# Kernel optimization log

Measured on AMD Instinct MI355X. Metric: run time of the kernel, lower is better.

Reference implementation:

```python
import jax, jax.numpy as jnp
import numpy as np

B, N, E, FIMG = 8, 10242, 61440, 512


def setup_inputs() -> dict:
    key = jax.random.key(0)
    ks = jax.random.split(key, 16)
    inp = {
        "batch_vertices": jax.random.normal(ks[0], (B, N, 3), jnp.float32),
        "img_features": jax.random.normal(ks[1], (B, FIMG), jnp.float32),
        "edge_indices": jax.random.randint(ks[2], (2, E), 0, N, dtype=jnp.int32),
    }
    dims = [(3 + FIMG, 512), (512, 512), (512, 512), (512, 512), (512, 64), (64, 3)]
    for i, (fi, fo) in enumerate(dims, 1):
        inp[f"W{i}"] = jax.random.normal(ks[2 + i], (fi, fo), jnp.float32) / np.sqrt(fi).astype(np.float32)
        inp[f"b{i}"] = jnp.zeros((fo,), jnp.float32)
    return inp


def _gcn(x, W, b, src, dst, norm, n):
    # GCNConv: h = x @ W ; out[i] = sum_{(j->i)} norm_e * h[j] ; + b
    h = jnp.einsum('bnf,fo->bno', x, W)
    msg = h[:, src, :] * norm[None, :, None]        # [B, E+N, Fo]
    out = jnp.zeros((x.shape[0], n, W.shape[1]), x.dtype).at[:, dst, :].add(msg)
    return out + b


def reference(batch_vertices, img_features, edge_indices,
              W1, b1, W2, b2, W3, b3, W4, b4, W5, b5, W6, b6):
    n = batch_vertices.shape[1]
    loop = jnp.arange(n, dtype=edge_indices.dtype)
    src = jnp.concatenate([edge_indices[0], loop])  # add self-loops (GCN)
    dst = jnp.concatenate([edge_indices[1], loop])
    deg = jnp.zeros((n,), jnp.float32).at[dst].add(1.0)
    dinv = jnp.where(deg > 0, jax.lax.rsqrt(deg), 0.0)
    norm = dinv[src] * dinv[dst]                    # symmetric normalization

    feat = jnp.broadcast_to(img_features[:, None, :], (batch_vertices.shape[0], n, img_features.shape[1]))
    x = jnp.concatenate([batch_vertices, feat], axis=2)

    x = _gcn(x, W1, b1, src, dst, norm, n)
    x = _gcn(x, W2, b2, src, dst, norm, n)
    x = jax.nn.relu(x)
    x = _gcn(x, W3, b3, src, dst, norm, n)
    x = _gcn(x, W4, b4, src, dst, norm, n)
    x = jax.nn.relu(x)
    x = _gcn(x, W5, b5, src, dst, norm, n)
    x = _gcn(x, W6, b6, src, dst, norm, n)
    return x
```

## Files before the change

kernel.cpp:

```cpp
#include <hip/hip_runtime.h>
#include <hip/hip_bf16.h>

typedef __attribute__((ext_vector_type(8))) short short8_t;
typedef __attribute__((ext_vector_type(4))) float f32x4;

#define DEV __device__ __forceinline__

constexpr int BB = 8;
constexpr int NV = 10242;
constexpr int NE = 61440;
constexpr int MROWS = BB * NV;
constexpr int KD = 512;

DEV float bf2f(ushort u) { union { unsigned i; float f; } v; v.i = ((unsigned)u) << 16; return v.f; }
DEV ushort f2bf(float f) {
    union { unsigned i; float f; } v; v.f = f;
    unsigned b = v.i;
    b += 0x7fffu + ((b >> 16) & 1u);
    return (ushort)(b >> 16);
}

__global__ void k_init(int* deg, int* fill) {
    int i = blockIdx.x * 256 + threadIdx.x;
    if (i < NV) { deg[i] = 1; fill[i] = 0; }
}

__global__ void k_count(const int* __restrict__ ei, int* __restrict__ deg) {
    int e = blockIdx.x * 256 + threadIdx.x;
    if (e < NE) atomicAdd(&deg[ei[NE + e]], 1);
}

__global__ __launch_bounds__(1024) void k_scan(const int* __restrict__ cnt, int* __restrict__ rp) {
    __shared__ int part[1024];
    const int t = threadIdx.x;
    const int chunk = (NV + 1023) / 1024;
    int b0 = t * chunk, b1 = min(b0 + chunk, NV);
    int s = 0;
    for (int i = b0; i < b1; ++i) s += cnt[i];
    part[t] = s;
    __syncthreads();
    for (int off = 1; off < 1024; off <<= 1) {
        int v = (t >= off) ? part[t - off] : 0;
        __syncthreads();
        part[t] += v;
        __syncthreads();
    }
    int run = (t == 0) ? 0 : part[t - 1];
    for (int i = b0; i < b1; ++i) { rp[i] = run; run += cnt[i]; }
    if (t == 1023) rp[NV] = part[1023];
}

__global__ void k_fill(const int* __restrict__ ei, const int* __restrict__ rp,
                       int* __restrict__ fill, const int* __restrict__ deg,
                       int* __restrict__ ci, float* __restrict__ val) {
    int e = blockIdx.x * 256 + threadIdx.x;
    if (e >= NE + NV) return;
    int s, d;
    if (e < NE) { s = ei[e]; d = ei[NE + e]; }
    else        { s = d = e - NE; }
    int p = atomicAdd(&fill[d], 1);
    int pos = rp[d] + p;
    ci[pos] = s;
    val[pos] = rsqrtf((float)deg[s]) * rsqrtf((float)deg[d]);
}

__global__ __launch_bounds__(256) void k_aggsc(const float* __restrict__ src, float* __restrict__ dst,
                                               const int* __restrict__ rp, const int* __restrict__ ci,
                                               const float* __restrict__ val,
                                               const float* __restrict__ sin, float* __restrict__ sout,
                                               int gMR_) {
    const int bid = blockIdx.x;
    if (bid < gMR_) {
        int idx = bid * 256 + threadIdx.x;
        if (idx >= MROWS) return;
        int b = idx / NV, i = idx - b * NV;
        float a0 = 0.f, a1 = 0.f, a2 = 0.f;
        const float* sb = src + (size_t)b * NV * 3;
        for (int e = rp[i]; e < rp[i + 1]; ++e) {
            int j = ci[e];
            float wv = val[e];
            a0 = fmaf(wv, sb[j * 3 + 0], a0);
            a1 = fmaf(wv, sb[j * 3 + 1], a1);
            a2 = fmaf(wv, sb[j * 3 + 2], a2);
        }
        float* o = dst + ((size_t)b * NV + i) * 3;
        o[0] = a0; o[1] = a1; o[2] = a2;
    } else {
        int i = (bid - gMR_) * 256 + threadIdx.x;
        if (i >= NV) return;
        float a = 0.f;
        if (sin) { for (int e = rp[i]; e < rp[i + 1]; ++e) a = fmaf(val[e], sin[ci[e]], a); }
        else     { for (int e = rp[i]; e < rp[i + 1]; ++e) a += val[e]; }
        sout[i] = a;
    }
}

__global__ __launch_bounds__(256) void k_prep(const float* __restrict__ W4, const float* __restrict__ W3,
                                              const float* __restrict__ W5, const float* __restrict__ W1,
                                              const float* __restrict__ b1, const float* __restrict__ b3,
                                              const float* __restrict__ W2, const float* __restrict__ img,
                                              ushort* __restrict__ Wt4, ushort* __restrict__ W3c,
                                              ushort* __restrict__ Wt5, float* __restrict__ CW12,
                                              float* __restrict__ b1w2, float* __restrict__ b3w4,
                                              float* __restrict__ basev) {
    constexpr int WB = (2 * 512 * 512 + 64 * 512) / 256;
    const int bid = blockIdx.x;
    const int t = threadIdx.x;
    if (bid < WB) {
        int idx = bid * 256 + t;
        if (idx < 512 * 512) {
            int n = idx >> 9, k = idx & 511;
            Wt4[idx] = f2bf(W4[k * 512 + n]);
        } else if (idx < 2 * 512 * 512) {
            int j = idx - 512 * 512;
            W3c[j] = f2bf(W3[j]);
        } else {
            int j = idx - 2 * 512 * 512;
            int n = j >> 9, k = j & 511;
            Wt5[j] = f2bf(W5[k * 64 + n]);
        }
    } else if (bid < WB + 10) {
        int r = bid - WB;
        int y = r >> 1;
        int c = (r & 1) * 256 + t;
        const float* Mrow = (y < 3) ? (W1 + y * 512) : (y == 3 ? b1 : b3);
        const float* W = (y < 4) ? W2 : W4;
        float a = 0.f;
        for (int k = 0; k < 512; ++k) a = fmaf(Mrow[k], W[(size_t)k * 512 + c], a);
        float* o = (y < 3) ? (CW12 + y * 512) : (y == 3 ? b1w2 : b3w4);
        o[c] = a;
    } else {
        int r = bid - (WB + 10);
        int b = r >> 1;
        int c = (r & 1) * 256 + t;
        float s = 0.f;
        for (int k = 0; k < 512; ++k) s = fmaf(img[b * 512 + k], W1[(size_t)(3 + k) * 512 + c], s);
        basev[b * 512 + c] = s;
    }
}

__global__ __launch_bounds__(128) void k_matvecs(const float* __restrict__ M, const float* __restrict__ W,
                                                 float* __restrict__ out) {
    int c = blockIdx.x * 128 + threadIdx.x;
    int r = blockIdx.y;
    float a = 0.f;
    for (int k = 0; k < 512; ++k) a = fmaf(M[r * 512 + k], W[(size_t)k * 512 + c], a);
    out[r * 512 + c] = a;
}

__global__ __launch_bounds__(256) void k_x2(const float* __restrict__ aggV2, const float* __restrict__ s,
                                            const float* __restrict__ s2, const float* __restrict__ CW12,
                                            const float* __restrict__ bw2, const float* __restrict__ b1w2,
                                            const float* __restrict__ b2, ushort* __restrict__ r2) {
    const int t = threadIdx.x;
    int row = blockIdx.x * 2 + (t >> 7);
    if (row >= MROWS) return;
    int i = row >> 3, b = row & 7;
    const float* av = aggV2 + ((size_t)b * NV + i) * 3;
    float a0 = av[0], a1 = av[1], a2 = av[2];
    float si = s[i], s2i = s2[i];
    int c = (t & 127) * 4;
    float4 w0 = *(const float4*)&CW12[c];
    float4 w1 = *(const float4*)&CW12[512 + c];
    float4 w2 = *(const float4*)&CW12[1024 + c];
    float4 bw = *(const float4*)&bw2[b * 512 + c];
    float4 bv = *(const float4*)&b1w2[c];
    float4 b2v = *(const float4*)&b2[c];
    float o0 = a0 * w0.x + a1 * w1.x + a2 * w2.x + s2i * bw.x + si * bv.x + b2v.x;
    float o1 = a0 * w0.y + a1 * w1.y + a2 * w2.y + s2i * bw.y + si * bv.y + b2v.y;
    float o2 = a0 * w0.z + a1 * w1.z + a2 * w2.z + s2i * bw.z + si * bv.z + b2v.z;
    float o3 = a0 * w0.w + a1 * w1.w + a2 * w2.w + s2i * bw.w + si * bv.w + b2v.w;
    ushort4 o;
    o.x = f2bf(fmaxf(o0, 0.f));
    o.y = f2bf(fmaxf(o1, 0.f));
    o.z = f2bf(fmaxf(o2, 0.f));
    o.w = f2bf(fmaxf(o3, 0.f));
    *(ushort4*)&r2[(size_t)row * 512 + c] = o;
}

#define WAITVM(n) do { \
    asm volatile("s_waitcnt vmcnt(" #n ")" ::: "memory"); \
    __builtin_amdgcn_sched_barrier(0); \
    __builtin_amdgcn_s_barrier(); \
    __builtin_amdgcn_sched_barrier(0); \
} while (0)

template <int EPI>
__global__ __launch_bounds__(256) void k_gemm(const ushort* __restrict__ A, const ushort* __restrict__ Bt,
                                              ushort* __restrict__ C, int Mr, int Nc,
                                              const float* __restrict__ sv, const float* __restrict__ eb1,
                                              const float* __restrict__ eb2) {
    const int ncb = (Nc + 127) >> 7;
    const int nrc = (Mr + 127) >> 7;
    const int cpx = (nrc + 7) >> 3;
    const int bid = blockIdx.x;
    const int xcd = bid & 7;
    const int k = bid >> 3;
    const int rc = xcd * cpx + k / ncb;
    const int cb = k % ncb;
    if (rc >= nrc) return;

    __shared__ __align__(16) ushort lA[3][4096];
    __shared__ __align__(16) ushort lB[3][4096];
    const int t = threadIdx.x;
    const int lane = t & 63, w = t >> 6;
    const int wr = w >> 1, wc = w & 1;
    const int r0 = rc * 128, c0 = cb * 128;

    const ushort* gA[2]; const ushort* gB[2];
    int ldsoff[2];
    #pragma unroll
    for (int i2 = 0; i2 < 2; ++i2) {
        int idx = i2 * 256 + t;
        int row = idx >> 2, slot = idx & 3;
        int srcslot = slot ^ ((row >> 1) & 3);
        int ar = min(r0 + row, Mr - 1);
        int bc = min(c0 + row, Nc - 1);
        gA[i2] = A + (size_t)ar * KD + srcslot * 8;
        gB[i2] = Bt + (size_t)bc * KD + srcslot * 8;
        ldsoff[i2] = idx * 8;
    }

    auto stage = [&](int buf, int kt) {
        int ko = kt * 32;
        #pragma unroll
        for (int i2 = 0; i2 < 2; ++i2) {
            __builtin_amdgcn_global_load_lds(
                (const __attribute__((address_space(1))) void*)(gA[i2] + ko),
                (__attribute__((address_space(3))) void*)(&lA[buf][ldsoff[i2]]), 16, 0, 0);
            __builtin_amdgcn_global_load_lds(
                (const __attribute__((address_space(1))) void*)(gB[i2] + ko),
                (__attribute__((address_space(3))) void*)(&lB[buf][ldsoff[i2]]), 16, 0, 0);
        }
    };

    f32x4 acc[4][4] = {};
    const int rloc = lane & 15;
    const int kb = lane >> 4;
    const int kbs = (kb ^ ((rloc >> 1) & 3)) * 8;

    auto compute = [&](int buf) {
        short8_t af[4], bfr[4];
        #pragma unroll
        for (int m = 0; m < 4; ++m) {
            af[m]  = *(const short8_t*)&lA[buf][(wr * 64 + m * 16 + rloc) * 32 + kbs];
            bfr[m] = *(const short8_t*)&lB[buf][(wc * 64 + m * 16 + rloc) * 32 + kbs];
        }
        #pragma unroll
        for (int m = 0; m < 4; ++m)
            #pragma unroll
            for (int n = 0; n < 4; ++n)
                acc[m][n] = __builtin_amdgcn_mfma_f32_16x16x32_bf16(bfr[n], af[m], acc[m][n], 0, 0, 0);
    };

    stage(0, 0);
    stage(1, 1);
    WAITVM(4);
    int cur = 0;
    for (int kt = 0; kt < 14; ++kt) {
        int sb = cur + 2; if (sb > 2) sb -= 3;
        stage(sb, kt + 2);
        compute(cur);
        WAITVM(4);
        cur = (cur == 2) ? 0 : cur + 1;
    }
    compute(cur);
    WAITVM(0);
    cur = (cur == 2) ? 0 : cur + 1;
    compute(cur);

    #pragma unroll
    for (int m = 0; m < 4; ++m) {
        const int gr = r0 + wr * 64 + m * 16 + rloc;
        if (gr >= Mr) continue;
        #pragma unroll
        for (int n = 0; n < 4; ++n) {
            const int qc = c0 + wc * 64 + n * 16;
            if (qc >= Nc) continue;
            const int gc = qc + kb * 4;
            float v0 = acc[m][n][0], v1 = acc[m][n][1], v2 = acc[m][n][2], v3 = acc[m][n][3];
            if (EPI == 1) {
                const float s = sv[gr >> 3];
                const float4 e1 = *(const float4*)&eb1[gc];
                const float4 e2 = *(const float4*)&eb2[gc];
                v0 = fmaxf(v0 + s * e1.x + e2.x, 0.f);
                v1 = fmaxf(v1 + s * e1.y + e2.y, 0.f);
                v2 = fmaxf(v2 + s * e1.z + e2.z, 0.f);
                v3 = fmaxf(v3 + s * e1.w + e2.w, 0.f);
            }
            ushort4 o;
            o.x = f2bf(v0); o.y = f2bf(v1); o.z = f2bf(v2); o.w = f2bf(v3);
            *(ushort4*)&C[(size_t)gr * Nc + gc] = o;
        }
    }
}

__global__ __launch_bounds__(256) void k_gemm64(const ushort* __restrict__ A, const ushort* __restrict__ Bt,
                                                ushort* __restrict__ C) {
    const int rc = blockIdx.x;
    const int r0 = rc * 256;
    __shared__ __align__(16) ushort lA[2][8192];
    __shared__ __align__(16) ushort lB[2][2048];
    const int t = threadIdx.x;
    const int lane = t & 63, w = t >> 6;

    const ushort* gA[4]; int loffA[4];
    #pragma unroll
    for (int p = 0; p < 4; ++p) {
        int idx = p * 256 + t;
        int row = idx >> 2, slot = idx & 3;
        int srcslot = slot ^ ((row >> 1) & 3);
        int ar = min(r0 + row, MROWS - 1);
        gA[p] = A + (size_t)ar * KD + srcslot * 8;
        loffA[p] = idx * 8;
    }
    const int brow = t >> 2, bslot = (t & 3) ^ ((brow >> 1) & 3);
    const ushort* gB = Bt + (size_t)brow * KD + bslot * 8;
    const int loffB = t * 8;

    auto stage = [&](int buf, int kt) {
        int ko = kt * 32;
        #pragma unroll
        for (int p = 0; p < 4; ++p)
            __builtin_amdgcn_global_load_lds(
                (const __attribute__((address_space(1))) void*)(gA[p] + ko),
                (__attribute__((address_space(3))) void*)(&lA[buf][loffA[p]]), 16, 0, 0);
        __builtin_amdgcn_global_load_lds(
            (const __attribute__((address_space(1))) void*)(gB + ko),
            (__attribute__((address_space(3))) void*)(&lB[buf][loffB]), 16, 0, 0);
    };

    f32x4 acc[4][4] = {};
    stage(0, 0);
    __syncthreads();
    int cur = 0;
    const int rloc = lane & 15;
    const int kb = lane >> 4;
    const int kbs = (kb ^ ((rloc >> 1) & 3)) * 8;
    for (int kt = 0; kt < 16; ++kt) {
        if (kt < 15) stage(cur ^ 1, kt + 1);
        short8_t af[4], bfr[4];
        #pragma unroll
        for (int m = 0; m < 4; ++m) {
            af[m]  = *(const short8_t*)&lA[cur][(w * 64 + m * 16 + rloc) * 32 + kbs];
            bfr[m] = *(const short8_t*)&lB[cur][(m * 16 + rloc) * 32 + kbs];
        }
        #pragma unroll
        for (int m = 0; m < 4; ++m)
            #pragma unroll
            for (int n = 0; n < 4; ++n)
                acc[m][n] = __builtin_amdgcn_mfma_f32_16x16x32_bf16(bfr[n], af[m], acc[m][n], 0, 0, 0);
        __syncthreads();
        cur ^= 1;
    }

    #pragma unroll
    for (int m = 0; m < 4; ++m) {
        const int gr = r0 + w * 64 + m * 16 + rloc;
        if (gr >= MROWS) continue;
        #pragma unroll
        for (int n = 0; n < 4; ++n) {
            const int gc = n * 16 + kb * 4;
            ushort4 o;
            o.x = f2bf(acc[m][n][0]); o.y = f2bf(acc[m][n][1]);
            o.z = f2bf(acc[m][n][2]); o.w = f2bf(acc[m][n][3]);
            *(ushort4*)&C[(size_t)gr * 64 + gc] = o;
        }
    }
}

template <bool RELU>
__global__ __launch_bounds__(512) void k_aggv(const ushort* __restrict__ h, ushort* __restrict__ xo,
                                              const int* __restrict__ rp, const int* __restrict__ ci,
                                              const float* __restrict__ val) {
    constexpr int CH = BB * 512;
    const int i = blockIdx.x;
    const int t = threadIdx.x;
    const int r0 = rp[i], r1 = rp[i + 1];
    const ushort* hb = h + t * 8;
    float acc[8] = {};
    for (int e = r0; e < r1; e += 4) {
        const bool p1 = e + 1 < r1, p2 = e + 2 < r1, p3 = e + 3 < r1;
        const int j0 = ci[e];
        const int j1 = p1 ? ci[e + 1] : j0;
        const int j2 = p2 ? ci[e + 2] : j0;
        const int j3 = p3 ? ci[e + 3] : j0;
        const float w0 = val[e];
        const float w1 = p1 ? val[e + 1] : 0.f;
        const float w2 = p2 ? val[e + 2] : 0.f;
        const float w3 = p3 ? val[e + 3] : 0.f;
        const short8_t v0 = *(const short8_t*)(hb + (size_t)j0 * CH);
        const short8_t v1 = *(const short8_t*)(hb + (size_t)j1 * CH);
        const short8_t v2 = *(const short8_t*)(hb + (size_t)j2 * CH);
        const short8_t v3 = *(const short8_t*)(hb + (size_t)j3 * CH);
        #pragma unroll
        for (int k = 0; k < 8; ++k) {
            float a = acc[k];
            a = fmaf(w0, bf2f((ushort)v0[k]), a);
            a = fmaf(w1, bf2f((ushort)v1[k]), a);
            a = fmaf(w2, bf2f((ushort)v2[k]), a);
            a = fmaf(w3, bf2f((ushort)v3[k]), a);
            acc[k] = a;
        }
    }
    short8_t o;
    #pragma unroll
    for (int k = 0; k < 8; ++k) {
        float a = acc[k];
        if (RELU) a = fmaxf(a, 0.f);
        o[k] = (short)f2bf(a);
    }
    *(short8_t*)(xo + (size_t)i * CH + t * 8) = o;
}

__global__ __launch_bounds__(64) void k_aggv64f(const ushort* __restrict__ h, float* __restrict__ h3,
                                                const int* __restrict__ rp, const int* __restrict__ ci,
                                                const float* __restrict__ val, const float* __restrict__ b5,
                                                const float* __restrict__ W6) {
    constexpr int CH = BB * 64;
    __shared__ float w6[192];
    const int t = threadIdx.x;
    w6[t] = W6[t]; w6[t + 64] = W6[t + 64]; w6[t + 128] = W6[t + 128];
    __syncthreads();
    const int i = blockIdx.x;
    const int r0 = rp[i], r1 = rp[i + 1];
    const ushort* hb = h + t * 8;
    float acc[8] = {};
    for (int e = r0; e < r1; e += 4) {
        const bool p1 = e + 1 < r1, p2 = e + 2 < r1, p3 = e + 3 < r1;
        const int j0 = ci[e];
        const int j1 = p1 ? ci[e + 1] : j0;
        const int j2 = p2 ? ci[e + 2] : j0;
        const int j3 = p3 ? ci[e + 3] : j0;
        const float w0 = val[e];
        const float w1 = p1 ? val[e + 1] : 0.f;
        const float w2 = p2 ? val[e + 2] : 0.f;
        const float w3 = p3 ? val[e + 3] : 0.f;
        const short8_t v0 = *(const short8_t*)(hb + (size_t)j0 * CH);
        const short8_t v1 = *(const short8_t*)(hb + (size_t)j1 * CH);
        const short8_t v2 = *(const short8_t*)(hb + (size_t)j2 * CH);
        const short8_t v3 = *(const short8_t*)(hb + (size_t)j3 * CH);
        #pragma unroll
        for (int k = 0; k < 8; ++k) {
            float a = acc[k];
            a = fmaf(w0, bf2f((ushort)v0[k]), a);
            a = fmaf(w1, bf2f((ushort)v1[k]), a);
            a = fmaf(w2, bf2f((ushort)v2[k]), a);
            a = fmaf(w3, bf2f((ushort)v3[k]), a);
            acc[k] = a;
        }
    }
    const int fb = (t & 7) * 8;
    float p0 = 0.f, p1 = 0.f, p2 = 0.f;
    #pragma unroll
    for (int k = 0; k < 8; ++k) {
        float a = acc[k] + b5[fb + k];
        p0 = fmaf(a, w6[(fb + k) * 3 + 0], p0);
        p1 = fmaf(a, w6[(fb + k) * 3 + 1], p1);
        p2 = fmaf(a, w6[(fb + k) * 3 + 2], p2);
    }
    p0 += __shfl_xor(p0, 1); p0 += __shfl_xor(p0, 2); p0 += __shfl_xor(p0, 4);
    p1 += __shfl_xor(p1, 1); p1 += __shfl_xor(p1, 2); p1 += __shfl_xor(p1, 4);
    p2 += __shfl_xor(p2, 1); p2 += __shfl_xor(p2, 2); p2 += __shfl_xor(p2, 4);
    if ((t & 7) == 0) {
        int row = i * 8 + (t >> 3);
        float* o = h3 + (size_t)row * 3;
        o[0] = p0; o[1] = p1; o[2] = p2;
    }
}

__global__ __launch_bounds__(256) void k_agg3(const float* __restrict__ h3, float* __restrict__ out,
                                              const int* __restrict__ rp, const int* __restrict__ ci,
                                              const float* __restrict__ val, const float* __restrict__ b6) {
    int idx = blockIdx.x * 256 + threadIdx.x;
    if (idx >= MROWS) return;
    int b = idx / NV, i = idx - b * NV;
    float a0 = b6[0], a1 = b6[1], a2 = b6[2];
    int r0 = rp[i], r1 = rp[i + 1];
    for (int e = r0; e < r1; ++e) {
        int j = ci[e];
        float wv = val[e];
        const float* hr = h3 + ((size_t)j * BB + b) * 3;
        a0 = fmaf(wv, hr[0], a0);
        a1 = fmaf(wv, hr[1], a1);
        a2 = fmaf(wv, hr[2], a2);
    }
    float* o = out + (size_t)idx * 3;
    o[0] = a0; o[1] = a1; o[2] = a2;
}

extern "C" void kernel_launch(void* const* d_in, const int* in_sizes, int n_in,
                              void* d_out, int out_size, void* d_ws, size_t ws_size,
                              hipStream_t stream) {
    const float* verts = (const float*)d_in[0];
    const float* img   = (const float*)d_in[1];
    const int*   ei    = (const int*)d_in[2];
    const float* W1 = (const float*)d_in[3];  const float* b1 = (const float*)d_in[4];
    const float* W2 = (const float*)d_in[5];  const float* b2 = (const float*)d_in[6];
    const float* W3 = (const float*)d_in[7];  const float* b3 = (const float*)d_in[8];
    const float* W4 = (const float*)d_in[9];  const float* b4 = (const float*)d_in[10];
    const float* W5 = (const float*)d_in[11]; const float* b5 = (const float*)d_in[12];
    const float* W6 = (const float*)d_in[13]; const float* b6 = (const float*)d_in[14];
    float* out = (float*)d_out;

    char* ws = (char*)d_ws;
    size_t off = 0;
    auto carve = [&](size_t bytes) -> void* {
        void* q = ws + off;
        off += (bytes + 255) & ~(size_t)255;
        return q;
    };
    ushort* bufA = (ushort*)carve((size_t)MROWS * 512 * 2);
    ushort* bufB = (ushort*)carve((size_t)MROWS * 512 * 2);
    ushort* Wt4  = (ushort*)carve((size_t)512 * 512 * 2);
    ushort* W3c  = (ushort*)carve((size_t)512 * 512 * 2);
    ushort* Wt34 = (ushort*)carve((size_t)512 * 512 * 2);
    ushort* Wt5  = (ushort*)carve((size_t)64 * 512 * 2);
    float*  basev = (float*)carve((size_t)BB * 512 * 4);
    float*  bw2   = (float*)carve((size_t)BB * 512 * 4);
    float*  CW12  = (float*)carve((size_t)3 * 512 * 4);
    float*  b1w2  = (float*)carve((size_t)512 * 4);
    float*  b3w4  = (float*)carve((size_t)512 * 4);
    int*    deg  = (int*)carve((size_t)NV * 4);
    int*    fill = (int*)carve((size_t)NV * 4);
    float*  sV   = (float*)carve((size_t)NV * 4);
    float*  s2V  = (float*)carve((size_t)NV * 4);
    int*    rp   = (int*)carve((size_t)(NV + 1) * 4);
    int*    ci   = (int*)carve((size_t)(NE + NV) * 4);
    float*  valv = (float*)carve((size_t)(NE + NV) * 4);
    float*  aggV  = (float*)carve((size_t)MROWS * 3 * 4);
    float*  aggV2 = (float*)carve((size_t)MROWS * 3 * 4);
    float*  h3   = (float*)carve((size_t)MROWS * 3 * 4);

    dim3 b256(256);
    const int gNV = (NV + 255) / 256;
    const int gMR = (MROWS + 255) / 256;
    k_init<<<dim3(gNV), b256, 0, stream>>>(deg, fill);
    k_count<<<dim3((NE + 255) / 256), b256, 0, stream>>>(ei, deg);
    k_scan<<<dim3(1), dim3(1024), 0, stream>>>(deg, rp);
    k_fill<<<dim3((NE + NV + 255) / 256), b256, 0, stream>>>(ei, rp, fill, deg, ci, valv);
    k_aggsc<<<dim3(gMR + gNV), b256, 0, stream>>>(verts, aggV, rp, ci, valv, nullptr, sV, gMR);
    k_aggsc<<<dim3(gMR + gNV), b256, 0, stream>>>(aggV, aggV2, rp, ci, valv, sV, s2V, gMR);
    k_prep<<<dim3(2176 + 10 + 16), b256, 0, stream>>>(W4, W3, W5, W1, b1, b3, W2, img,
                                                      Wt4, W3c, Wt5, CW12, b1w2, b3w4, basev);
    k_matvecs<<<dim3(4, BB), dim3(128), 0, stream>>>(basev, W2, bw2);
    k_gemm<0><<<dim3(32), b256, 0, stream>>>(Wt4, W3c, Wt34, 512, 512, nullptr, nullptr, nullptr);
    k_x2<<<dim3((MROWS + 1) / 2), b256, 0, stream>>>(aggV2, sV, s2V, CW12, bw2, b1w2, b2, bufA);
    k_aggv<false><<<dim3(NV), dim3(512), 0, stream>>>(bufA, bufB, rp, ci, valv);
    k_aggv<false><<<dim3(NV), dim3(512), 0, stream>>>(bufB, bufA, rp, ci, valv);
    const int nrc = (MROWS + 127) / 128;
    const int g512 = 8 * ((nrc + 7) / 8) * 4;
    k_gemm<1><<<dim3(g512), b256, 0, stream>>>(bufA, Wt34, bufB, MROWS, 512, sV, b3w4, b4);
    k_gemm64<<<dim3((MROWS + 255) / 256), b256, 0, stream>>>(bufB, Wt5, bufA);
    k_aggv64f<<<dim3(NV), dim3(64), 0, stream>>>(bufA, h3, rp, ci, valv, b5, W6);
    k_agg3<<<dim3(gMR), b256, 0, stream>>>(h3, out, rp, ci, valv, b6);
}
```

Baseline: 455.2 us.

## Split sparse aggregation into XCD-pinned column panels for L2 locality

Replaces the one-block-per-vertex 512-thread aggregation with 256-thread blocks that each handle 16 vertices over one 128-column panel of the 4096-wide row. Panels are assigned by block index modulo 8 so each XCD keeps working on the same column slice. The aim is for neighbor gathers to hit in that XCD's L2 instead of pulling full 8KB rows across all dies. Each vertex's CSR indices and weights are now read once per panel (32 times) instead of once, and per-vertex edge-loop divergence within a wave rises.

After: 391.4 us (median of 2 runs). -14.0%, faster.

```diff
diff --git a/kernel.cpp b/kernel.cpp
--- a/kernel.cpp
+++ b/kernel.cpp
@@ -9,6 +9,7 @@
 constexpr int BB = 8;
 constexpr int NV = 10242;
 constexpr int NE = 61440;
+constexpr int NET = NE + NV;
 constexpr int MROWS = BB * NV;
 constexpr int KD = 512;
 
@@ -54,7 +55,7 @@
                        int* __restrict__ fill, const int* __restrict__ deg,
                        int* __restrict__ ci, float* __restrict__ val) {
     int e = blockIdx.x * 256 + threadIdx.x;
-    if (e >= NE + NV) return;
+    if (e >= NET) return;
     int s, d;
     if (e < NE) { s = ei[e]; d = ei[NE + e]; }
     else        { s = d = e - NE; }
@@ -369,15 +370,22 @@
     }
 }
 
-template <bool RELU>
-__global__ __launch_bounds__(512) void k_aggv(const ushort* __restrict__ h, ushort* __restrict__ xo,
-                                              const int* __restrict__ rp, const int* __restrict__ ci,
-                                              const float* __restrict__ val) {
-    constexpr int CH = BB * 512;
-    const int i = blockIdx.x;
-    const int t = threadIdx.x;
+constexpr int NVG16 = (NV + 15) / 16;
+__global__ __launch_bounds__(256) void k_aggvp(const ushort* __restrict__ h, ushort* __restrict__ xo,
+                                               const int* __restrict__ rp, const int* __restrict__ ci,
+                                               const float* __restrict__ val) {
+    const int bid = blockIdx.x;
+    const int xcd = bid & 7;
+    const int g = bid >> 3;
+    const int round = g / NVG16;
+    const int vg = g - round * NVG16;
+    const int panel = xcd + round * 8;
+    const int t = threadIdx.x;
+    const int i = vg * 16 + (t >> 4);
+    if (i >= NV) return;
+    const int po = panel * 128 + (t & 15) * 8;
+    const ushort* hb = h + po;
     const int r0 = rp[i], r1 = rp[i + 1];
-    const ushort* hb = h + t * 8;
     float acc[8] = {};
     for (int e = r0; e < r1; e += 4) {
         const bool p1 = e + 1 < r1, p2 = e + 2 < r1, p3 = e + 3 < r1;
@@ -389,10 +397,10 @@
         const float w1 = p1 ? val[e + 1] : 0.f;
         const float w2 = p2 ? val[e + 2] : 0.f;
         const float w3 = p3 ? val[e + 3] : 0.f;
-        const short8_t v0 = *(const short8_t*)(hb + (size_t)j0 * CH);
-        const short8_t v1 = *(const short8_t*)(hb + (size_t)j1 * CH);
-        const short8_t v2 = *(const short8_t*)(hb + (size_t)j2 * CH);
-        const short8_t v3 = *(const short8_t*)(hb + (size_t)j3 * CH);
+        const short8_t v0 = *(const short8_t*)(hb + (size_t)j0 * 4096);
+        const short8_t v1 = *(const short8_t*)(hb + (size_t)j1 * 4096);
+        const short8_t v2 = *(const short8_t*)(hb + (size_t)j2 * 4096);
+        const short8_t v3 = *(const short8_t*)(hb + (size_t)j3 * 4096);
         #pragma unroll
         for (int k = 0; k < 8; ++k) {
             float a = acc[k];
@@ -405,12 +413,8 @@
     }
     short8_t o;
     #pragma unroll
-    for (int k = 0; k < 8; ++k) {
-        float a = acc[k];
-        if (RELU) a = fmaxf(a, 0.f);
-        o[k] = (short)f2bf(a);
-    }
-    *(short8_t*)(xo + (size_t)i * CH + t * 8) = o;
+    for (int k = 0; k < 8; ++k) o[k] = (short)f2bf(acc[k]);
+    *(short8_t*)(xo + (size_t)i * 4096 + po) = o;
 }
 
 __global__ __launch_bounds__(64) void k_aggv64f(const ushort* __restrict__ h, float* __restrict__ h3,
@@ -526,8 +530,8 @@
     float*  sV   = (float*)carve((size_t)NV * 4);
     float*  s2V  = (float*)carve((size_t)NV * 4);
     int*    rp   = (int*)carve((size_t)(NV + 1) * 4);
-    int*    ci   = (int*)carve((size_t)(NE + NV) * 4);
-    float*  valv = (float*)carve((size_t)(NE + NV) * 4);
+    int*    ci   = (int*)carve((size_t)NET * 4);
+    float*  valv = (float*)carve((size_t)NET * 4);
     float*  aggV  = (float*)carve((size_t)MROWS * 3 * 4);
     float*  aggV2 = (float*)carve((size_t)MROWS * 3 * 4);
     float*  h3   = (float*)carve((size_t)MROWS * 3 * 4);
@@ -538,7 +542,7 @@
     k_init<<<dim3(gNV), b256, 0, stream>>>(deg, fill);
     k_count<<<dim3((NE + 255) / 256), b256, 0, stream>>>(ei, deg);
     k_scan<<<dim3(1), dim3(1024), 0, stream>>>(deg, rp);
-    k_fill<<<dim3((NE + NV + 255) / 256), b256, 0, stream>>>(ei, rp, fill, deg, ci, valv);
+    k_fill<<<dim3((NET + 255) / 256), b256, 0, stream>>>(ei, rp, fill, deg, ci, valv);
     k_aggsc<<<dim3(gMR + gNV), b256, 0, stream>>>(verts, aggV, rp, ci, valv, nullptr, sV, gMR);
     k_aggsc<<<dim3(gMR + gNV), b256, 0, stream>>>(aggV, aggV2, rp, ci, valv, sV, s2V, gMR);
     k_prep<<<dim3(2176 + 10 + 16), b256, 0, stream>>>(W4, W3, W5, W1, b1, b3, W2, img,
@@ -546,8 +550,9 @@
     k_matvecs<<<dim3(4, BB), dim3(128), 0, stream>>>(basev, W2, bw2);
     k_gemm<0><<<dim3(32), b256, 0, stream>>>(Wt4, W3c, Wt34, 512, 512, nullptr, nullptr, nullptr);
     k_x2<<<dim3((MROWS + 1) / 2), b256, 0, stream>>>(aggV2, sV, s2V, CW12, bw2, b1w2, b2, bufA);
-    k_aggv<false><<<dim3(NV), dim3(512), 0, stream>>>(bufA, bufB, rp, ci, valv);
-    k_aggv<false><<<dim3(NV), dim3(512), 0, stream>>>(bufB, bufA, rp, ci, valv);
+    const int gP = 8 * 4 * NVG16;
+    k_aggvp<<<dim3(gP), b256, 0, stream>>>(bufA, bufB, rp, ci, valv);
+    k_aggvp<<<dim3(gP), b256, 0, stream>>>(bufB, bufA, rp, ci, valv);
     const int nrc = (MROWS + 127) / 128;
     const int g512 = 8 * ((nrc + 7) / 8) * 4;
     k_gemm<1><<<dim3(g512), b256, 0, stream>>>(bufA, Wt34, bufB, MROWS, 512, sV, b3w4, b4);
```
